# Kernel optimization log

Measured on AMD Instinct MI355X. Metric: run time of the kernel, lower is better.

Reference implementation:

```python
import jax, jax.numpy as jnp
import numpy as np

B, D, H = 16384, 64, 256

def setup_inputs() -> dict:
    key = jax.random.key(0)
    ks = jax.random.split(key, 24)
    s = 0.05
    inp = {
        'x':   jax.random.normal(ks[0], (B, D), dtype=jnp.float32),
        # stacked per-feature MLPs (torch ModuleList of Linear(1,H)->ReLU->Linear(H,H)->ReLU->Linear(H,1))
        'W1':  jax.random.normal(ks[1], (D, H), dtype=jnp.float32) * s,      # in=1
        'b1':  jax.random.normal(ks[2], (D, H), dtype=jnp.float32) * s,
        'W2':  jax.random.normal(ks[3], (D, H, H), dtype=jnp.float32) * s,
        'b2':  jax.random.normal(ks[4], (D, H), dtype=jnp.float32) * s,
        'W3':  jax.random.normal(ks[5], (D, H), dtype=jnp.float32) * s,      # out=1
        'b3':  jax.random.normal(ks[6], (D,), dtype=jnp.float32) * s,
        # attention fusion
        'Wq':  jax.random.normal(ks[7], (H, D), dtype=jnp.float32) * s,
        'bq':  jax.random.normal(ks[8], (H,), dtype=jnp.float32) * s,
        'Wk':  jax.random.normal(ks[9], (H, D), dtype=jnp.float32) * s,
        'bk':  jax.random.normal(ks[10], (H,), dtype=jnp.float32) * s,
        'Ws':  jax.random.normal(ks[11], (D, H), dtype=jnp.float32) * s,
        'bs':  jax.random.normal(ks[12], (D,), dtype=jnp.float32) * s,
        # cross MLP: Linear(D,H)->ReLU->Linear(H,1)
        'Wc1': jax.random.normal(ks[13], (H, D), dtype=jnp.float32) * s,
        'bc1': jax.random.normal(ks[14], (H,), dtype=jnp.float32) * s,
        'Wc2': jax.random.normal(ks[15], (H,), dtype=jnp.float32) * s,
        'bc2': jax.random.normal(ks[16], (1,), dtype=jnp.float32) * s,
        # g_func: Linear(1,H)->ReLU->Linear(H,1)
        'Wg1': jax.random.normal(ks[17], (H,), dtype=jnp.float32) * s,
        'bg1': jax.random.normal(ks[18], (H,), dtype=jnp.float32) * s,
        'Wg2': jax.random.normal(ks[19], (H,), dtype=jnp.float32) * s,
        'bg2': jax.random.normal(ks[20], (1,), dtype=jnp.float32) * s,
    }
    return inp

def reference(x, W1, b1, W2, b2, W3, b3, Wq, bq, Wk, bk, Ws, bs,
              Wc1, bc1, Wc2, bc2, Wg1, bg1, Wg2, bg2):
    # per-feature 3-layer MLPs, vectorized over the feature axis d
    a1 = jax.nn.relu(x[:, :, None] * W1[None] + b1[None])           # [B, D, H]
    a2 = jax.nn.relu(jnp.einsum('bdh,dhk->bdk', a1, W2) + b2[None]) # [B, D, H]
    h_cat = jnp.einsum('bdh,dh->bd', a2, W3) + b3[None]             # [B, D]
    # tiny tanh-softmax attention fusion
    q = h_cat @ Wq.T + bq                                           # [B, H]
    k = h_cat @ Wk.T + bk                                           # [B, H]
    scores = jnp.tanh(q * k) @ Ws.T + bs                            # [B, D]
    wts = jax.nn.softmax(scores, axis=1)
    weighted = jnp.sum(h_cat * wts, axis=1, keepdims=True)          # [B, 1]
    cross = jax.nn.relu(h_cat @ Wc1.T + bc1) @ Wc2[:, None] + bc2   # [B, 1]
    comb = weighted + cross                                         # [B, 1]
    out = jax.nn.relu(comb * Wg1[None] + bg1[None]) @ Wg2[:, None] + bg2  # [B, 1]
    return out
```

## Files before the change

### kernel.cpp

```cpp
#include <hip/hip_runtime.h>
#include <stdint.h>

#define Bn 16384
#define Dn 64
#define Hn 256

typedef short bf16x8 __attribute__((ext_vector_type(8)));
typedef float f32x2 __attribute__((ext_vector_type(2)));
typedef float f32x4 __attribute__((ext_vector_type(4)));
typedef float f32x16 __attribute__((ext_vector_type(16)));

__device__ __forceinline__ unsigned f2bf1(float f) {
  unsigned u = __float_as_uint(f);
  return (u + 0x7FFFu + ((u >> 16) & 1u)) >> 16;
}

__global__ __launch_bounds__(256) void pack_w2(const float* __restrict__ W2,
                                               unsigned short* __restrict__ Bp) {
  int gidx = blockIdx.x * 4 + (threadIdx.x >> 6);
  int lane = threadIdx.x & 63;
  int d  = gidx >> 7;
  int s  = (gidx >> 3) & 15;
  int nb = gidx & 7;
  int k0 = s * 16 + ((lane >> 5) << 3);
  int n  = (nb << 5) + (lane & 31);
  const float* src = W2 + ((size_t)d * Hn + k0) * Hn + n;
  unsigned t[8];
  #pragma unroll
  for (int b = 0; b < 8; ++b) t[b] = f2bf1(src[(size_t)b * Hn]);
  uint4 w;
  w.x = t[0] | (t[1] << 16);
  w.y = t[2] | (t[3] << 16);
  w.z = t[4] | (t[5] << 16);
  w.w = t[6] | (t[7] << 16);
  size_t off = (((size_t)gidx) * 64 + lane) * 8;
  *(uint4*)(Bp + off) = w;
}

__global__ __launch_bounds__(256) void prep_t(
    const float* __restrict__ Wq, const float* __restrict__ Wk,
    const float* __restrict__ Wc1, const float* __restrict__ Ws,
    float* __restrict__ WqT, float* __restrict__ WkT,
    float* __restrict__ Wc1T, float* __restrict__ WsT) {
  int t = blockIdx.x * 256 + threadIdx.x;
  int h = t >> 6, dd = t & 63;
  WqT[dd * 256 + h]  = Wq[h * 64 + dd];
  WkT[dd * 256 + h]  = Wk[h * 64 + dd];
  Wc1T[dd * 256 + h] = Wc1[h * 64 + dd];
  WsT[h * 64 + dd]   = Ws[dd * 256 + h];
}

__global__ __launch_bounds__(512, 1) void gemm_hcat(
    const float* __restrict__ x, const float* __restrict__ W1,
    const float* __restrict__ b1, const float* __restrict__ b2,
    const float* __restrict__ W3, const float* __restrict__ b3,
    const unsigned short* __restrict__ Bp, float* __restrict__ hcT) {
  __shared__ char Bs[131072];

  int bid = blockIdx.x;
  int xcd = bid & 7;
  int dl = (bid >> 3) & 7;
  int chunk = bid >> 6;
  int d = xcd * 8 + dl;
  int base = chunk * 4096;

  int tid = threadIdx.x;
  int lane = tid & 63;
  int w = tid >> 6;
  int l31 = lane & 31;
  int hsel = lane >> 5;

  const unsigned short* BpD = Bp + (size_t)d * 65536;
  const float* W1d = W1 + d * Hn;
  const float* b1d = b1 + d * Hn;
  const float* b2d = b2 + d * Hn;
  const float* W3d = W3 + d * Hn;
  float b3d = b3[d];

  #pragma unroll
  for (int i = 0; i < 16; ++i) {
    int idx = i * 512 + tid;
    const void* g = (const void*)(BpD + (size_t)idx * 8);
    void* l = (void*)(Bs + (size_t)idx * 16);
    __builtin_amdgcn_global_load_lds((const __attribute__((address_space(1))) void*)g,
                                     (__attribute__((address_space(3))) void*)l, 16, 0, 0);
  }
  __syncthreads();

  for (int pr = w; pr < 64; pr += 8) {
    int row0 = base + pr * 64 + l31;
    int row1 = row0 + 32;
    float xv0 = x[(size_t)row0 * Dn + d];
    float xv1 = x[(size_t)row1 * Dn + d];

    bf16x8 af0[16], af1[16];
    #pragma unroll
    for (int s = 0; s < 16; ++s) {
      int k = s * 16 + (hsel << 3);
      const f32x2* w1p = (const f32x2*)(W1d + k);
      const f32x2* b1p = (const f32x2*)(b1d + k);
      f32x2 wv0 = w1p[0], wv1 = w1p[1], wv2 = w1p[2], wv3 = w1p[3];
      f32x2 bv0 = b1p[0], bv1 = b1p[1], bv2 = b1p[2], bv3 = b1p[3];
      f32x2 z = {0.f, 0.f};
      {
        f32x2 xr = {xv0, xv0};
        f32x2 p0 = __builtin_elementwise_max(xr * wv0 + bv0, z);
        f32x2 p1 = __builtin_elementwise_max(xr * wv1 + bv1, z);
        f32x2 p2 = __builtin_elementwise_max(xr * wv2 + bv2, z);
        f32x2 p3 = __builtin_elementwise_max(xr * wv3 + bv3, z);
        union { uint4 u; bf16x8 v; } pk;
        asm("v_cvt_pk_bf16_f32 %0, %1, %2" : "=v"(pk.u.x) : "v"(p0.x), "v"(p0.y));
        asm("v_cvt_pk_bf16_f32 %0, %1, %2" : "=v"(pk.u.y) : "v"(p1.x), "v"(p1.y));
        asm("v_cvt_pk_bf16_f32 %0, %1, %2" : "=v"(pk.u.z) : "v"(p2.x), "v"(p2.y));
        asm("v_cvt_pk_bf16_f32 %0, %1, %2" : "=v"(pk.u.w) : "v"(p3.x), "v"(p3.y));
        af0[s] = pk.v;
      }
      {
        f32x2 xr = {xv1, xv1};
        f32x2 p0 = __builtin_elementwise_max(xr * wv0 + bv0, z);
        f32x2 p1 = __builtin_elementwise_max(xr * wv1 + bv1, z);
        f32x2 p2 = __builtin_elementwise_max(xr * wv2 + bv2, z);
        f32x2 p3 = __builtin_elementwise_max(xr * wv3 + bv3, z);
        union { uint4 u; bf16x8 v; } pk;
        asm("v_cvt_pk_bf16_f32 %0, %1, %2" : "=v"(pk.u.x) : "v"(p0.x), "v"(p0.y));
        asm("v_cvt_pk_bf16_f32 %0, %1, %2" : "=v"(pk.u.y) : "v"(p1.x), "v"(p1.y));
        asm("v_cvt_pk_bf16_f32 %0, %1, %2" : "=v"(pk.u.z) : "v"(p2.x), "v"(p2.y));
        asm("v_cvt_pk_bf16_f32 %0, %1, %2" : "=v"(pk.u.w) : "v"(p3.x), "v"(p3.y));
        af1[s] = pk.v;
      }
    }

    float ph0 = 0.f, ph1 = 0.f;
    #pragma unroll 1
    for (int nb = 0; nb < 8; ++nb) {
      int cb = (nb << 5) + (hsel << 2);

      f32x16 acc0a, acc1a, acc0b, acc1b;
      #pragma unroll
      for (int q = 0; q < 4; ++q) {
        float4 bv = *(const float4*)(b2d + cb + (q << 3));
        acc0a[4 * q + 0] = bv.x; acc1a[4 * q + 0] = bv.x;
        acc0a[4 * q + 1] = bv.y; acc1a[4 * q + 1] = bv.y;
        acc0a[4 * q + 2] = bv.z; acc1a[4 * q + 2] = bv.z;
        acc0a[4 * q + 3] = bv.w; acc1a[4 * q + 3] = bv.w;
        acc0b[4 * q + 0] = 0.f; acc1b[4 * q + 0] = 0.f;
        acc0b[4 * q + 1] = 0.f; acc1b[4 * q + 1] = 0.f;
        acc0b[4 * q + 2] = 0.f; acc1b[4 * q + 2] = 0.f;
        acc0b[4 * q + 3] = 0.f; acc1b[4 * q + 3] = 0.f;
      }

      __builtin_amdgcn_s_setprio(1);
      #pragma unroll
      for (int s = 0; s < 16; s += 2) {
        bf16x8 bfe = *(const bf16x8*)(Bs + ((((s << 3) + nb) << 6) + lane) * 16);
        acc0a = __builtin_amdgcn_mfma_f32_32x32x16_bf16(bfe, af0[s], acc0a, 0, 0, 0);
        acc1a = __builtin_amdgcn_mfma_f32_32x32x16_bf16(bfe, af1[s], acc1a, 0, 0, 0);
        bf16x8 bfo = *(const bf16x8*)(Bs + (((((s + 1) << 3) + nb) << 6) + lane) * 16);
        acc0b = __builtin_amdgcn_mfma_f32_32x32x16_bf16(bfo, af0[s + 1], acc0b, 0, 0, 0);
        acc1b = __builtin_amdgcn_mfma_f32_32x32x16_bf16(bfo, af1[s + 1], acc1b, 0, 0, 0);
      }
      __builtin_amdgcn_s_setprio(0);

      #pragma unroll
      for (int q = 0; q < 4; ++q) {
        float4 wv = *(const float4*)(W3d + cb + (q << 3));
        ph0 = fmaf(fmaxf(acc0a[4 * q + 0] + acc0b[4 * q + 0], 0.f), wv.x, ph0);
        ph0 = fmaf(fmaxf(acc0a[4 * q + 1] + acc0b[4 * q + 1], 0.f), wv.y, ph0);
        ph0 = fmaf(fmaxf(acc0a[4 * q + 2] + acc0b[4 * q + 2], 0.f), wv.z, ph0);
        ph0 = fmaf(fmaxf(acc0a[4 * q + 3] + acc0b[4 * q + 3], 0.f), wv.w, ph0);
        ph1 = fmaf(fmaxf(acc1a[4 * q + 0] + acc1b[4 * q + 0], 0.f), wv.x, ph1);
        ph1 = fmaf(fmaxf(acc1a[4 * q + 1] + acc1b[4 * q + 1], 0.f), wv.y, ph1);
        ph1 = fmaf(fmaxf(acc1a[4 * q + 2] + acc1b[4 * q + 2], 0.f), wv.z, ph1);
        ph1 = fmaf(fmaxf(acc1a[4 * q + 3] + acc1b[4 * q + 3], 0.f), wv.w, ph1);
      }
    }

    ph0 += __shfl_xor(ph0, 32);
    ph1 += __shfl_xor(ph1, 32);
    if (lane < 32) {
      hcT[(size_t)d * Bn + row0] = ph0 + b3d;
      hcT[(size_t)d * Bn + row1] = ph1 + b3d;
    }
  }
}

__global__ __launch_bounds__(256) void fused_tail(
    const float* __restrict__ hcT, const float* __restrict__ WqT,
    const float* __restrict__ bq, const float* __restrict__ WkT,
    const float* __restrict__ bk, const float* __restrict__ WsT,
    const float* __restrict__ bs, const float* __restrict__ Wc1T,
    const float* __restrict__ bc1, const float* __restrict__ Wc2,
    const float* __restrict__ bc2, const float* __restrict__ Wg1,
    const float* __restrict__ bg1, const float* __restrict__ Wg2,
    const float* __restrict__ bg2, float* __restrict__ out) {
  __shared__ float hcs[4][4][64];
  __shared__ float ts[4][4][256];
  int wid = threadIdx.x >> 6;
  int lane = threadIdx.x & 63;
  int r0 = (blockIdx.x * 4 + wid) * 4;
  float4 hc4 = *(const float4*)(hcT + (size_t)lane * Bn + r0);
  hcs[wid][0][lane] = hc4.x;
  hcs[wid][1][lane] = hc4.y;
  hcs[wid][2][lane] = hc4.z;
  hcs[wid][3][lane] = hc4.w;
  __syncthreads();

  float qv[4][4], kv[4][4], cv[4][4];
  #pragma unroll
  for (int j = 0; j < 4; ++j) {
    int h = lane + 64 * j;
    float bqv = bq[h], bkv = bk[h], bcv = bc1[h];
    #pragma unroll
    for (int r = 0; r < 4; ++r) { qv[r][j] = bqv; kv[r][j] = bkv; cv[r][j] = bcv; }
  }
  for (int d2 = 0; d2 < 64; ++d2) {
    float hv0 = hcs[wid][0][d2], hv1 = hcs[wid][1][d2];
    float hv2 = hcs[wid][2][d2], hv3 = hcs[wid][3][d2];
    #pragma unroll
    for (int j = 0; j < 4; ++j) {
      int h = lane + 64 * j;
      float wq = WqT[d2 * 256 + h], wk = WkT[d2 * 256 + h], wc = Wc1T[d2 * 256 + h];
      qv[0][j] = fmaf(wq, hv0, qv[0][j]); qv[1][j] = fmaf(wq, hv1, qv[1][j]);
      qv[2][j] = fmaf(wq, hv2, qv[2][j]); qv[3][j] = fmaf(wq, hv3, qv[3][j]);
      kv[0][j] = fmaf(wk, hv0, kv[0][j]); kv[1][j] = fmaf(wk, hv1, kv[1][j]);
      kv[2][j] = fmaf(wk, hv2, kv[2][j]); kv[3][j] = fmaf(wk, hv3, kv[3][j]);
      cv[0][j] = fmaf(wc, hv0, cv[0][j]); cv[1][j] = fmaf(wc, hv1, cv[1][j]);
      cv[2][j] = fmaf(wc, hv2, cv[2][j]); cv[3][j] = fmaf(wc, hv3, cv[3][j]);
    }
  }
  #pragma unroll
  for (int r = 0; r < 4; ++r)
    #pragma unroll
    for (int j = 0; j < 4; ++j)
      ts[wid][r][lane + 64 * j] = tanhf(qv[r][j] * kv[r][j]);
  __syncthreads();

  float sc[4];
  { float b = bs[lane]; sc[0] = b; sc[1] = b; sc[2] = b; sc[3] = b; }
  for (int h2 = 0; h2 < 256; ++h2) {
    float w = WsT[h2 * 64 + lane];
    sc[0] = fmaf(w, ts[wid][0][h2], sc[0]);
    sc[1] = fmaf(w, ts[wid][1][h2], sc[1]);
    sc[2] = fmaf(w, ts[wid][2][h2], sc[2]);
    sc[3] = fmaf(w, ts[wid][3][h2], sc[3]);
  }

  float hcr[4] = {hc4.x, hc4.y, hc4.z, hc4.w};
  float res[4];
  #pragma unroll
  for (int r = 0; r < 4; ++r) {
    float s = sc[r];
    float mx = s;
    #pragma unroll
    for (int off = 1; off < 64; off <<= 1) mx = fmaxf(mx, __shfl_xor(mx, off));
    float e = __expf(s - mx);
    float se = e;
    #pragma unroll
    for (int off = 1; off < 64; off <<= 1) se += __shfl_xor(se, off);
    float wgt = hcr[r] * (e / se);
    #pragma unroll
    for (int off = 1; off < 64; off <<= 1) wgt += __shfl_xor(wgt, off);
    float cp = 0.f;
    #pragma unroll
    for (int j = 0; j < 4; ++j) cp = fmaf(fmaxf(cv[r][j], 0.f), Wc2[lane + 64 * j], cp);
    #pragma unroll
    for (int off = 1; off < 64; off <<= 1) cp += __shfl_xor(cp, off);
    float comb = wgt + cp + bc2[0];
    float fp = 0.f;
    #pragma unroll
    for (int j = 0; j < 4; ++j) {
      int h = lane + 64 * j;
      fp = fmaf(fmaxf(fmaf(comb, Wg1[h], bg1[h]), 0.f), Wg2[h], fp);
    }
    #pragma unroll
    for (int off = 1; off < 64; off <<= 1) fp += __shfl_xor(fp, off);
    res[r] = fp + bg2[0];
  }
  if (lane == 0) {
    float4 o = make_float4(res[0], res[1], res[2], res[3]);
    *(float4*)(out + r0) = o;
  }
}

extern "C" void kernel_launch(void* const* d_in, const int* in_sizes, int n_in,
                              void* d_out, int out_size, void* d_ws, size_t ws_size,
                              hipStream_t stream) {
  const float* x   = (const float*)d_in[0];
  const float* W1  = (const float*)d_in[1];
  const float* b1  = (const float*)d_in[2];
  const float* W2  = (const float*)d_in[3];
  const float* b2  = (const float*)d_in[4];
  const float* W3  = (const float*)d_in[5];
  const float* b3  = (const float*)d_in[6];
  const float* Wq  = (const float*)d_in[7];
  const float* bq  = (const float*)d_in[8];
  const float* Wk  = (const float*)d_in[9];
  const float* bk  = (const float*)d_in[10];
  const float* Ws  = (const float*)d_in[11];
  const float* bs  = (const float*)d_in[12];
  const float* Wc1 = (const float*)d_in[13];
  const float* bc1 = (const float*)d_in[14];
  const float* Wc2 = (const float*)d_in[15];
  const float* bc2 = (const float*)d_in[16];
  const float* Wg1 = (const float*)d_in[17];
  const float* bg1 = (const float*)d_in[18];
  const float* Wg2 = (const float*)d_in[19];
  const float* bg2 = (const float*)d_in[20];

  unsigned short* Bp = (unsigned short*)d_ws;
  float* hcT  = (float*)((char*)d_ws + 8388608);
  float* WqT  = (float*)((char*)d_ws + 12582912);
  float* WkT  = WqT + 16384;
  float* Wc1T = WkT + 16384;
  float* WsT  = Wc1T + 16384;

  pack_w2<<<2048, 256, 0, stream>>>(W2, Bp);
  prep_t<<<64, 256, 0, stream>>>(Wq, Wk, Wc1, Ws, WqT, WkT, Wc1T, WsT);
  gemm_hcat<<<256, 512, 0, stream>>>(x, W1, b1, b2, W3, b3, Bp, hcT);
  fused_tail<<<1024, 256, 0, stream>>>(hcT, WqT, bq, WkT, bk, WsT, bs, Wc1T, bc1,
                                       Wc2, bc2, Wg1, bg1, Wg2, bg2, (float*)d_out);
}
```

Baseline: 178.4 us.

## Raise GEMM block to 12 waves, drop split accumulators, merge pack kernels

The main GEMM kernel goes from 512 to 768 threads per block, and its row-pair loop now strides by 12 waves, so more waves per CU can hide MFMA and LDS latency. To free registers for the larger block, the two split accumulators (even/odd k) are collapsed into one, which makes each MFMA chain fully serial. The W2 bf16 packing and weight-transpose kernels are merged into one launch to save a kernel launch. The 64 row pairs no longer divide evenly across waves, and about 170 VGPRs per wave is tight for the bf16 fragments, so spilling is a risk.

```diff
diff --git a/kernel.cpp b/kernel.cpp
--- a/kernel.cpp
+++ b/kernel.cpp
@@ -15,42 +15,42 @@
   return (u + 0x7FFFu + ((u >> 16) & 1u)) >> 16;
 }
 
-__global__ __launch_bounds__(256) void pack_w2(const float* __restrict__ W2,
-                                               unsigned short* __restrict__ Bp) {
-  int gidx = blockIdx.x * 4 + (threadIdx.x >> 6);
-  int lane = threadIdx.x & 63;
-  int d  = gidx >> 7;
-  int s  = (gidx >> 3) & 15;
-  int nb = gidx & 7;
-  int k0 = s * 16 + ((lane >> 5) << 3);
-  int n  = (nb << 5) + (lane & 31);
-  const float* src = W2 + ((size_t)d * Hn + k0) * Hn + n;
-  unsigned t[8];
-  #pragma unroll
-  for (int b = 0; b < 8; ++b) t[b] = f2bf1(src[(size_t)b * Hn]);
-  uint4 w;
-  w.x = t[0] | (t[1] << 16);
-  w.y = t[2] | (t[3] << 16);
-  w.z = t[4] | (t[5] << 16);
-  w.w = t[6] | (t[7] << 16);
-  size_t off = (((size_t)gidx) * 64 + lane) * 8;
-  *(uint4*)(Bp + off) = w;
-}
-
-__global__ __launch_bounds__(256) void prep_t(
+__global__ __launch_bounds__(256) void pack_all(
+    const float* __restrict__ W2, unsigned short* __restrict__ Bp,
     const float* __restrict__ Wq, const float* __restrict__ Wk,
     const float* __restrict__ Wc1, const float* __restrict__ Ws,
     float* __restrict__ WqT, float* __restrict__ WkT,
     float* __restrict__ Wc1T, float* __restrict__ WsT) {
-  int t = blockIdx.x * 256 + threadIdx.x;
-  int h = t >> 6, dd = t & 63;
-  WqT[dd * 256 + h]  = Wq[h * 64 + dd];
-  WkT[dd * 256 + h]  = Wk[h * 64 + dd];
-  Wc1T[dd * 256 + h] = Wc1[h * 64 + dd];
-  WsT[h * 64 + dd]   = Ws[dd * 256 + h];
-}
-
-__global__ __launch_bounds__(512, 1) void gemm_hcat(
+  if (blockIdx.x < 2048) {
+    int gidx = blockIdx.x * 4 + (threadIdx.x >> 6);
+    int lane = threadIdx.x & 63;
+    int d  = gidx >> 7;
+    int s  = (gidx >> 3) & 15;
+    int nb = gidx & 7;
+    int k0 = s * 16 + ((lane >> 5) << 3);
+    int n  = (nb << 5) + (lane & 31);
+    const float* src = W2 + ((size_t)d * Hn + k0) * Hn + n;
+    unsigned t[8];
+    #pragma unroll
+    for (int b = 0; b < 8; ++b) t[b] = f2bf1(src[(size_t)b * Hn]);
+    uint4 w;
+    w.x = t[0] | (t[1] << 16);
+    w.y = t[2] | (t[3] << 16);
+    w.z = t[4] | (t[5] << 16);
+    w.w = t[6] | (t[7] << 16);
+    size_t off = (((size_t)gidx) * 64 + lane) * 8;
+    *(uint4*)(Bp + off) = w;
+  } else {
+    int t = (blockIdx.x - 2048) * 256 + threadIdx.x;
+    int h = t >> 6, dd = t & 63;
+    WqT[dd * 256 + h]  = Wq[h * 64 + dd];
+    WkT[dd * 256 + h]  = Wk[h * 64 + dd];
+    Wc1T[dd * 256 + h] = Wc1[h * 64 + dd];
+    WsT[h * 64 + dd]   = Ws[dd * 256 + h];
+  }
+}
+
+__global__ __launch_bounds__(768, 1) void gemm_hcat(
     const float* __restrict__ x, const float* __restrict__ W1,
     const float* __restrict__ b1, const float* __restrict__ b2,
     const float* __restrict__ W3, const float* __restrict__ b3,
@@ -78,16 +78,18 @@
   float b3d = b3[d];
 
   #pragma unroll
-  for (int i = 0; i < 16; ++i) {
-    int idx = i * 512 + tid;
-    const void* g = (const void*)(BpD + (size_t)idx * 8);
-    void* l = (void*)(Bs + (size_t)idx * 16);
-    __builtin_amdgcn_global_load_lds((const __attribute__((address_space(1))) void*)g,
-                                     (__attribute__((address_space(3))) void*)l, 16, 0, 0);
+  for (int i = 0; i < 11; ++i) {
+    int idx = i * 768 + tid;
+    if (idx < 8192) {
+      const void* g = (const void*)(BpD + (size_t)idx * 8);
+      void* l = (void*)(Bs + (size_t)idx * 16);
+      __builtin_amdgcn_global_load_lds((const __attribute__((address_space(1))) void*)g,
+                                       (__attribute__((address_space(3))) void*)l, 16, 0, 0);
+    }
   }
   __syncthreads();
 
-  for (int pr = w; pr < 64; pr += 8) {
+  for (int pr = w; pr < 64; pr += 12) {
     int row0 = base + pr * 64 + l31;
     int row1 = row0 + 32;
     float xv0 = x[(size_t)row0 * Dn + d];
@@ -135,43 +137,36 @@
     for (int nb = 0; nb < 8; ++nb) {
       int cb = (nb << 5) + (hsel << 2);
 
-      f32x16 acc0a, acc1a, acc0b, acc1b;
+      f32x16 acc0, acc1;
       #pragma unroll
       for (int q = 0; q < 4; ++q) {
         float4 bv = *(const float4*)(b2d + cb + (q << 3));
-        acc0a[4 * q + 0] = bv.x; acc1a[4 * q + 0] = bv.x;
-        acc0a[4 * q + 1] = bv.y; acc1a[4 * q + 1] = bv.y;
-        acc0a[4 * q + 2] = bv.z; acc1a[4 * q + 2] = bv.z;
-        acc0a[4 * q + 3] = bv.w; acc1a[4 * q + 3] = bv.w;
-        acc0b[4 * q + 0] = 0.f; acc1b[4 * q + 0] = 0.f;
-        acc0b[4 * q + 1] = 0.f; acc1b[4 * q + 1] = 0.f;
-        acc0b[4 * q + 2] = 0.f; acc1b[4 * q + 2] = 0.f;
-        acc0b[4 * q + 3] = 0.f; acc1b[4 * q + 3] = 0.f;
+        acc0[4 * q + 0] = bv.x; acc1[4 * q + 0] = bv.x;
+        acc0[4 * q + 1] = bv.y; acc1[4 * q + 1] = bv.y;
+        acc0[4 * q + 2] = bv.z; acc1[4 * q + 2] = bv.z;
+        acc0[4 * q + 3] = bv.w; acc1[4 * q + 3] = bv.w;
       }
 
       __builtin_amdgcn_s_setprio(1);
       #pragma unroll
-      for (int s = 0; s < 16; s += 2) {
-        bf16x8 bfe = *(const bf16x8*)(Bs + ((((s << 3) + nb) << 6) + lane) * 16);
-        acc0a = __builtin_amdgcn_mfma_f32_32x32x16_bf16(bfe, af0[s], acc0a, 0, 0, 0);
-        acc1a = __builtin_amdgcn_mfma_f32_32x32x16_bf16(bfe, af1[s], acc1a, 0, 0, 0);
-        bf16x8 bfo = *(const bf16x8*)(Bs + (((((s + 1) << 3) + nb) << 6) + lane) * 16);
-        acc0b = __builtin_amdgcn_mfma_f32_32x32x16_bf16(bfo, af0[s + 1], acc0b, 0, 0, 0);
-        acc1b = __builtin_amdgcn_mfma_f32_32x32x16_bf16(bfo, af1[s + 1], acc1b, 0, 0, 0);
+      for (int s = 0; s < 16; ++s) {
+        bf16x8 bfr = *(const bf16x8*)(Bs + ((((s << 3) + nb) << 6) + lane) * 16);
+        acc0 = __builtin_amdgcn_mfma_f32_32x32x16_bf16(bfr, af0[s], acc0, 0, 0, 0);
+        acc1 = __builtin_amdgcn_mfma_f32_32x32x16_bf16(bfr, af1[s], acc1, 0, 0, 0);
       }
       __builtin_amdgcn_s_setprio(0);
 
       #pragma unroll
       for (int q = 0; q < 4; ++q) {
         float4 wv = *(const float4*)(W3d + cb + (q << 3));
-        ph0 = fmaf(fmaxf(acc0a[4 * q + 0] + acc0b[4 * q + 0], 0.f), wv.x, ph0);
-        ph0 = fmaf(fmaxf(acc0a[4 * q + 1] + acc0b[4 * q + 1], 0.f), wv.y, ph0);
-        ph0 = fmaf(fmaxf(acc0a[4 * q + 2] + acc0b[4 * q + 2], 0.f), wv.z, ph0);
-        ph0 = fmaf(fmaxf(acc0a[4 * q + 3] + acc0b[4 * q + 3], 0.f), wv.w, ph0);
-        ph1 = fmaf(fmaxf(acc1a[4 * q + 0] + acc1b[4 * q + 0], 0.f), wv.x, ph1);
-        ph1 = fmaf(fmaxf(acc1a[4 * q + 1] + acc1b[4 * q + 1], 0.f), wv.y, ph1);
-        ph1 = fmaf(fmaxf(acc1a[4 * q + 2] + acc1b[4 * q + 2], 0.f), wv.z, ph1);
-        ph1 = fmaf(fmaxf(acc1a[4 * q + 3] + acc1b[4 * q + 3], 0.f), wv.w, ph1);
+        ph0 = fmaf(fmaxf(acc0[4 * q + 0], 0.f), wv.x, ph0);
+        ph0 = fmaf(fmaxf(acc0[4 * q + 1], 0.f), wv.y, ph0);
+        ph0 = fmaf(fmaxf(acc0[4 * q + 2], 0.f), wv.z, ph0);
+        ph0 = fmaf(fmaxf(acc0[4 * q + 3], 0.f), wv.w, ph0);
+        ph1 = fmaf(fmaxf(acc1[4 * q + 0], 0.f), wv.x, ph1);
+        ph1 = fmaf(fmaxf(acc1[4 * q + 1], 0.f), wv.y, ph1);
+        ph1 = fmaf(fmaxf(acc1[4 * q + 2], 0.f), wv.z, ph1);
+        ph1 = fmaf(fmaxf(acc1[4 * q + 3], 0.f), wv.w, ph1);
       }
     }
 
@@ -314,9 +309,8 @@
   float* Wc1T = WkT + 16384;
   float* WsT  = Wc1T + 16384;
 
-  pack_w2<<<2048, 256, 0, stream>>>(W2, Bp);
-  prep_t<<<64, 256, 0, stream>>>(Wq, Wk, Wc1, Ws, WqT, WkT, Wc1T, WsT);
-  gemm_hcat<<<256, 512, 0, stream>>>(x, W1, b1, b2, W3, b3, Bp, hcT);
+  pack_all<<<2112, 256, 0, stream>>>(W2, Bp, Wq, Wk, Wc1, Ws, WqT, WkT, Wc1T, WsT);
+  gemm_hcat<<<256, 768, 0, stream>>>(x, W1, b1, b2, W3, b3, Bp, hcT);
   fused_tail<<<1024, 256, 0, stream>>>(hcT, WqT, bq, WkT, bk, WsT, bs, Wc1T, bc1,
                                        Wc2, bc2, Wg1, bg1, Wg2, bg2, (float*)d_out);
 }
```

New measurement: 216.8 us. 1.22x slower.
